# Optimization experiments

Hardware: AMD Instinct MI355X
Metric: run time of the kernel (lower is better)

Reference implementation:

```python
import jax, jax.numpy as jnp
import numpy as np

N, C, HI, WI = 8, 3, 512, 512   # src_img NCHW (input_img_size)
HO, WO = 2048, 2048             # output canvas (output_img_size[2:])
EPS = 1e-8


def _transform_one(img, coor_row):
    """Replicates: sigmoid box params -> theta -> F.affine_grid -> F.grid_sample
    (bilinear, zeros padding, align_corners=False). Theta has zero off-diagonals,
    so the grid is separable in x/y and the bilinear sample factorizes.
    img: [C, HI, WI]; coor_row: [4]. Returns (sample [C,HO,WO], mask [HO,WO])."""
    x = jax.nn.sigmoid(coor_row[0]) * WO
    y = jax.nn.sigmoid(coor_row[1]) * HO
    w = jax.nn.sigmoid(coor_row[2]) * WO
    h = jax.nn.sigmoid(coor_row[3]) * HO
    a = WO / (w + EPS)
    tx = 2.0 / WO * (WO / 2.0 - x) * a
    b = HO / (h + EPS)
    ty = 2.0 / HO * (HO / 2.0 - y) * b
    # affine_grid base coords (align_corners=False): center-of-pixel normalized
    xs = (2.0 * jnp.arange(WO, dtype=img.dtype) + 1.0) / WO - 1.0
    ys = (2.0 * jnp.arange(HO, dtype=img.dtype) + 1.0) / HO - 1.0
    gx = a * xs + tx          # [WO]
    gy = b * ys + ty          # [HO]
    # grid_sample unnormalize (align_corners=False)
    ix = ((gx + 1.0) * WI - 1.0) / 2.0
    iy = ((gy + 1.0) * HI - 1.0) / 2.0
    x0f = jnp.floor(ix); y0f = jnp.floor(iy)
    wx1 = ix - x0f; wx0 = 1.0 - wx1
    wy1 = iy - y0f; wy0 = 1.0 - wy1
    x0 = x0f.astype(jnp.int32); x1 = x0 + 1
    y0 = y0f.astype(jnp.int32); y1 = y0 + 1
    vx0 = ((x0 >= 0) & (x0 < WI)).astype(img.dtype)
    vx1 = ((x1 >= 0) & (x1 < WI)).astype(img.dtype)
    vy0 = ((y0 >= 0) & (y0 < HI)).astype(img.dtype)
    vy1 = ((y1 >= 0) & (y1 < HI)).astype(img.dtype)
    x0c = jnp.clip(x0, 0, WI - 1); x1c = jnp.clip(x1, 0, WI - 1)
    y0c = jnp.clip(y0, 0, HI - 1); y1c = jnp.clip(y1, 0, HI - 1)
    wyv0 = wy0 * vy0; wyv1 = wy1 * vy1
    wxv0 = wx0 * vx0; wxv1 = wx1 * vx1
    # separable bilinear gather with zero padding
    rows = img[:, y0c, :] * wyv0[None, :, None] + img[:, y1c, :] * wyv1[None, :, None]  # [C,HO,WI]
    samp = rows[:, :, x0c] * wxv0[None, None, :] + rows[:, :, x1c] * wxv1[None, None, :]  # [C,HO,WO]
    # grid_sample of an all-ones mask == sum of in-bounds bilinear weights (separable)
    mask = (wyv0 + wyv1)[:, None] * (wxv0 + wxv1)[None, :]  # [HO,WO]
    return samp, mask


def _composite(src_img, bg_img, coor):
    def step(bg, inp):
        img, c = inp
        s, m = _transform_one(img, c)
        bg = bg * (1.0 - m)[None, None] + (s * m[None])[None]
        return bg, None
    bg, _ = jax.lax.scan(step, bg_img, (src_img, coor))
    return bg


def setup_inputs() -> dict:
    key = jax.random.key(0)
    k1, k2, k3 = jax.random.split(key, 3)
    src_img = jax.random.normal(k1, (N, C, HI, WI), dtype=jnp.float32)
    bg_img = jax.random.uniform(k2, (1, C, HO, WO), dtype=jnp.float32)
    coor = jax.random.normal(k3, (N, 4), dtype=jnp.float32)  # nn.Parameter
    return {"src_img": src_img, "bg_img": bg_img, "coor": coor}


def reference(src_img, bg_img, coor):
    return _composite(src_img, bg_img, coor)
```

## Files before the change

kernel.cpp:

```cpp
#include <hip/hip_runtime.h>

#define WI 512
#define HI 512
#define WO 2048
#define HO 2048
#define NIMG 8
#define CCH 3
#define EPS 1e-8f
#define PLANE (HI * WI)

#define SEG  512
#define TPB  128
#define PXT  4
#define MAXR 516

struct ImgUni {
    float wy0, wy1, my;
    int   y0o, y1o;
    int   t0, t1;
};

__device__ __forceinline__ bool img_uniforms(const float4 P, const float ys,
                                             const int wo0, ImgUni& u) {
    const float gy  = P.z * ys + P.w;
    const float iy  = ((gy + 1.0f) * (float)HI - 1.0f) * 0.5f;
    const float y0f = floorf(iy);
    const float fy1 = iy - y0f;
    const float fy0 = 1.0f - fy1;
    const float y1f = y0f + 1.0f;
    const float v0  = (y0f >= 0.0f && y0f < (float)HI) ? 1.0f : 0.0f;
    const float v1  = (y1f >= 0.0f && y1f < (float)HI) ? 1.0f : 0.0f;
    u.wy0 = fy0 * v0;
    u.wy1 = fy1 * v1;
    u.my  = u.wy0 + u.wy1;
    u.y0o = (int)fminf(fmaxf(y0f, 0.0f), (float)(HI - 1)) * WI;
    u.y1o = (int)fminf(fmaxf(y1f, 0.0f), (float)(HI - 1)) * WI;
    if (!(u.my > 0.0f)) return false;

    const float a  = P.x, tx = P.y;
    const float xsf = (2.0f * (float)wo0 + 1.0f) / (float)WO - 1.0f;
    const float xsl = (2.0f * (float)(wo0 + SEG - 1) + 1.0f) / (float)WO - 1.0f;
    const float ixf = ((a * xsf + tx + 1.0f) * (float)WI - 1.0f) * 0.5f;
    const float ixl = ((a * xsl + tx + 1.0f) * (float)WI - 1.0f) * 0.5f;
    if (ixl <= -1.0f || ixf >= (float)WI) return false;
    u.t0 = (int)fminf(fmaxf(floorf(ixf), 0.0f), (float)(WI - 1));
    u.t1 = (int)fminf(fmaxf(floorf(ixl) + 1.0f, 0.0f), (float)(WI - 1));
    return true;
}

__launch_bounds__(TPB)
__global__ void diffcomp_fused7(const float* __restrict__ src,
                                const float* __restrict__ bg,
                                const float* __restrict__ coor,
                                float* __restrict__ out) {
    __shared__ float  cs[2][CCH][MAXR];
    __shared__ float4 prm[NIMG];

    const int tid = threadIdx.x;
    const int b   = blockIdx.x;
    const int row = b >> 2;
    const int wo0 = (b & 3) * SEG;

    if (tid < NIMG) {
        const float cx  = coor[tid * 4 + 0];
        const float cy  = coor[tid * 4 + 1];
        const float cw  = coor[tid * 4 + 2];
        const float chh = coor[tid * 4 + 3];
        const float x = (1.0f / (1.0f + expf(-cx))) * (float)WO;
        const float y = (1.0f / (1.0f + expf(-cy))) * (float)HO;
        const float w = (1.0f / (1.0f + expf(-cw))) * (float)WO;
        const float h = (1.0f / (1.0f + expf(-chh))) * (float)HO;
        const float a  = (float)WO / (w + EPS);
        const float tx = (2.0f / (float)WO) * ((float)WO * 0.5f - x) * a;
        const float bb = (float)HO / (h + EPS);
        const float ty = (2.0f / (float)HO) * ((float)HO * 0.5f - y) * bb;
        prm[tid] = make_float4(a, tx, bb, ty);
    }
    __syncthreads();

    const float ys = (2.0f * (float)row + 1.0f) / (float)HO - 1.0f;

    unsigned cov = 0u;
#pragma unroll
    for (int n = 0; n < NIMG; n++) {
        ImgUni u;
        if (img_uniforms(prm[n], ys, wo0, u)) cov |= (1u << n);
    }

    const int base = row * WO + wo0 + tid;
    float acc[CCH][PXT];
#pragma unroll
    for (int c = 0; c < CCH; c++)
#pragma unroll
        for (int p = 0; p < PXT; p++)
            acc[c][p] = bg[c * HO * WO + base + p * TPB];

    if (cov) {
        auto stage = [&](int slot, int n) {
            ImgUni u;
            img_uniforms(prm[n], ys, wo0, u);
            const float* ib = src + n * (CCH * PLANE);
            const int R = u.t1 - u.t0 + 1;
            for (int i = tid; i < R; i += TPB) {
#pragma unroll
                for (int c = 0; c < CCH; c++) {
                    const float r0 = ib[c * PLANE + u.y0o + u.t0 + i];
                    const float r1 = ib[c * PLANE + u.y1o + u.t0 + i];
                    cs[slot][c][i] = r0 * u.wy0 + r1 * u.wy1;
                }
            }
        };

        auto blend = [&](int slot, int n) {
            ImgUni u;
            img_uniforms(prm[n], ys, wo0, u);
            const float a  = prm[n].x;
            const float tx = prm[n].y;
            const int lim = u.t1 - u.t0;
#pragma unroll
            for (int p = 0; p < PXT; p++) {
                const int wo = wo0 + p * TPB + tid;
                const float xs  = (2.0f * (float)wo + 1.0f) / (float)WO - 1.0f;
                const float gx  = a * xs + tx;
                const float ix  = ((gx + 1.0f) * (float)WI - 1.0f) * 0.5f;
                const float x0f = floorf(ix);
                const float fx1 = ix - x0f;
                const float fx0 = 1.0f - fx1;
                const float x1f = x0f + 1.0f;
                const float v0  = (x0f >= 0.0f && x0f < (float)WI) ? 1.0f : 0.0f;
                const float v1  = (x1f >= 0.0f && x1f < (float)WI) ? 1.0f : 0.0f;
                const float wx0 = fx0 * v0;
                const float wx1 = fx1 * v1;
                int x0r = (int)fminf(fmaxf(x0f, 0.0f), (float)(WI - 1)) - u.t0;
                int x1r = (int)fminf(fmaxf(x1f, 0.0f), (float)(WI - 1)) - u.t0;
                x0r = min(max(x0r, 0), lim);
                x1r = min(max(x1r, 0), lim);
                const float m  = u.my * (wx0 + wx1);
                const float om = 1.0f - m;
#pragma unroll
                for (int c = 0; c < CCH; c++) {
                    const float q0 = cs[slot][c][x0r];
                    const float q1 = cs[slot][c][x1r];
                    const float sc = q0 * wx0 + q1 * wx1;
                    acc[c][p] = acc[c][p] * om + sc * m;
                }
            }
        };

        int cur = (int)__builtin_ctz(cov);
        unsigned rest = cov & (cov - 1u);

        stage(0, cur);
        __syncthreads();

        int s = 0;
        while (true) {
            const int nxt = rest ? (int)__builtin_ctz(rest) : -1;
            if (nxt >= 0) stage(s ^ 1, nxt);
            blend(s, cur);
            __syncthreads();
            if (nxt < 0) break;
            cur = nxt;
            rest &= rest - 1u;
            s ^= 1;
        }
    }

#pragma unroll
    for (int c = 0; c < CCH; c++)
#pragma unroll
        for (int p = 0; p < PXT; p++)
            out[c * HO * WO + base + p * TPB] = acc[c][p];
}

extern "C" void kernel_launch(void* const* d_in, const int* in_sizes, int n_in,
                              void* d_out, int out_size, void* d_ws, size_t ws_size,
                              hipStream_t stream) {
    const float* src  = (const float*)d_in[0];
    const float* bg   = (const float*)d_in[1];
    const float* coor = (const float*)d_in[2];
    float* out = (float*)d_out;
    (void)d_ws; (void)ws_size;

    hipLaunchKernelGGL(diffcomp_fused7, dim3(HO * 4), dim3(TPB), 0, stream,
                       src, bg, coor, out);
}
```

Baseline: 151.6 us.

## Prefetch source rows into registers with float4 loads and widen blocks to half-rows

Each block now covers 1024 output pixels with 256 threads instead of 512 with 128. Source-row staging uses 16-byte aligned float4 loads into registers, and the next image's rows are prefetched while the current image is committed and blended. The column x-coordinates are precomputed once per thread. This aims to cut global-load instruction count and hide load latency, at the cost of more registers and a wider, 4-aligned staging window. There is also a possible race: a slot is rewritten in the next iteration while other threads may still be blending from it, since there is no barrier after the blend.

After: 134.3 us. 11.4% less time.

```diff
diff --git a/kernel.cpp b/kernel.cpp
--- a/kernel.cpp
+++ b/kernel.cpp
@@ -9,19 +9,21 @@
 #define EPS 1e-8f
 #define PLANE (HI * WI)
 
-#define SEG  512
-#define TPB  128
+#define TPB  256
+#define SEG  1024
 #define PXT  4
-#define MAXR 516
-
-struct ImgUni {
+#define CAP  520
+
+struct SState {
     float wy0, wy1, my;
-    int   y0o, y1o;
-    int   t0, t1;
+    int   t0a, R, lim;
+    int   valid;
 };
 
-__device__ __forceinline__ bool img_uniforms(const float4 P, const float ys,
-                                             const int wo0, ImgUni& u) {
+__device__ __forceinline__ SState calc_state(const float4 P, const float ys,
+                                             const int wo0) {
+    SState st; st.valid = 0; st.wy0 = st.wy1 = st.my = 0.0f;
+    st.t0a = 0; st.R = 0; st.lim = 0;
     const float gy  = P.z * ys + P.w;
     const float iy  = ((gy + 1.0f) * (float)HI - 1.0f) * 0.5f;
     const float y0f = floorf(iy);
@@ -30,36 +32,41 @@
     const float y1f = y0f + 1.0f;
     const float v0  = (y0f >= 0.0f && y0f < (float)HI) ? 1.0f : 0.0f;
     const float v1  = (y1f >= 0.0f && y1f < (float)HI) ? 1.0f : 0.0f;
-    u.wy0 = fy0 * v0;
-    u.wy1 = fy1 * v1;
-    u.my  = u.wy0 + u.wy1;
-    u.y0o = (int)fminf(fmaxf(y0f, 0.0f), (float)(HI - 1)) * WI;
-    u.y1o = (int)fminf(fmaxf(y1f, 0.0f), (float)(HI - 1)) * WI;
-    if (!(u.my > 0.0f)) return false;
+    st.wy0 = fy0 * v0;
+    st.wy1 = fy1 * v1;
+    st.my  = st.wy0 + st.wy1;
+    if (!(st.my > 0.0f)) return st;
 
     const float a  = P.x, tx = P.y;
     const float xsf = (2.0f * (float)wo0 + 1.0f) / (float)WO - 1.0f;
     const float xsl = (2.0f * (float)(wo0 + SEG - 1) + 1.0f) / (float)WO - 1.0f;
     const float ixf = ((a * xsf + tx + 1.0f) * (float)WI - 1.0f) * 0.5f;
     const float ixl = ((a * xsl + tx + 1.0f) * (float)WI - 1.0f) * 0.5f;
-    if (ixl <= -1.0f || ixf >= (float)WI) return false;
-    u.t0 = (int)fminf(fmaxf(floorf(ixf), 0.0f), (float)(WI - 1));
-    u.t1 = (int)fminf(fmaxf(floorf(ixl) + 1.0f, 0.0f), (float)(WI - 1));
-    return true;
+    if (ixl <= -1.0f || ixf >= (float)WI) return st;
+
+    const int t0 = (int)fminf(fmaxf(floorf(ixf), 0.0f), (float)(WI - 1));
+    const int t1 = (int)fminf(fmaxf(floorf(ixl) + 1.0f, 0.0f), (float)(WI - 1));
+    st.t0a = t0 & ~3;
+    int R = (t1 - st.t0a + 4) & ~3;
+    if (R > WI - st.t0a) R = WI - st.t0a;
+    st.R   = R;
+    st.lim = t1 - st.t0a;
+    st.valid = 1;
+    return st;
 }
 
 __launch_bounds__(TPB)
-__global__ void diffcomp_fused7(const float* __restrict__ src,
-                                const float* __restrict__ bg,
-                                const float* __restrict__ coor,
-                                float* __restrict__ out) {
-    __shared__ float  cs[2][CCH][MAXR];
+__global__ void diffcomp_v8(const float* __restrict__ src,
+                            const float* __restrict__ bg,
+                            const float* __restrict__ coor,
+                            float* __restrict__ out) {
+    __shared__ float  cs[2][CCH][CAP];
     __shared__ float4 prm[NIMG];
 
     const int tid = threadIdx.x;
     const int b   = blockIdx.x;
-    const int row = b >> 2;
-    const int wo0 = (b & 3) * SEG;
+    const int row = b >> 1;
+    const int wo0 = (b & 1) << 10;
 
     if (tid < NIMG) {
         const float cx  = coor[tid * 4 + 0];
@@ -83,8 +90,14 @@
     unsigned cov = 0u;
 #pragma unroll
     for (int n = 0; n < NIMG; n++) {
-        ImgUni u;
-        if (img_uniforms(prm[n], ys, wo0, u)) cov |= (1u << n);
+        if (calc_state(prm[n], ys, wo0).valid) cov |= (1u << n);
+    }
+
+    float xsv[PXT];
+#pragma unroll
+    for (int p = 0; p < PXT; p++) {
+        const int wo = wo0 + p * TPB + tid;
+        xsv[p] = (2.0f * (float)wo + 1.0f) / (float)WO - 1.0f;
     }
 
     const int base = row * WO + wo0 + tid;
@@ -96,32 +109,49 @@
             acc[c][p] = bg[c * HO * WO + base + p * TPB];
 
     if (cov) {
-        auto stage = [&](int slot, int n) {
-            ImgUni u;
-            img_uniforms(prm[n], ys, wo0, u);
-            const float* ib = src + n * (CCH * PLANE);
-            const int R = u.t1 - u.t0 + 1;
-            for (int i = tid; i < R; i += TPB) {
+        float4 A0[CCH], A1[CCH], B0[CCH], B1[CCH];
+        SState stA, stB;
+
+        auto load_img = [&](int n, SState& st, float4* r0, float4* r1) {
+            st = calc_state(prm[n], ys, wo0);
+            const int xo = tid << 2;
+            if (xo < st.R) {
+                const float* ib = src + n * (CCH * PLANE) + st.t0a + xo;
+                const float gy  = prm[n].z * ys + prm[n].w;
+                const float iy  = ((gy + 1.0f) * (float)HI - 1.0f) * 0.5f;
+                const float y0f = floorf(iy);
+                const int y0o = (int)fminf(fmaxf(y0f, 0.0f), (float)(HI - 1)) * WI;
+                const int y1o = (int)fminf(fmaxf(y0f + 1.0f, 0.0f), (float)(HI - 1)) * WI;
 #pragma unroll
                 for (int c = 0; c < CCH; c++) {
-                    const float r0 = ib[c * PLANE + u.y0o + u.t0 + i];
-                    const float r1 = ib[c * PLANE + u.y1o + u.t0 + i];
-                    cs[slot][c][i] = r0 * u.wy0 + r1 * u.wy1;
+                    r0[c] = *(const float4*)(ib + c * PLANE + y0o);
+                    r1[c] = *(const float4*)(ib + c * PLANE + y1o);
                 }
             }
         };
 
-        auto blend = [&](int slot, int n) {
-            ImgUni u;
-            img_uniforms(prm[n], ys, wo0, u);
+        auto commit_img = [&](int slot, const SState& st,
+                              const float4* r0, const float4* r1) {
+            const int xo = tid << 2;
+            if (xo < st.R) {
+#pragma unroll
+                for (int c = 0; c < CCH; c++) {
+                    float4 rc;
+                    rc.x = r0[c].x * st.wy0 + r1[c].x * st.wy1;
+                    rc.y = r0[c].y * st.wy0 + r1[c].y * st.wy1;
+                    rc.z = r0[c].z * st.wy0 + r1[c].z * st.wy1;
+                    rc.w = r0[c].w * st.wy0 + r1[c].w * st.wy1;
+                    *(float4*)&cs[slot][c][xo] = rc;
+                }
+            }
+        };
+
+        auto blend_img = [&](int slot, int n, const SState& st) {
             const float a  = prm[n].x;
             const float tx = prm[n].y;
-            const int lim = u.t1 - u.t0;
 #pragma unroll
             for (int p = 0; p < PXT; p++) {
-                const int wo = wo0 + p * TPB + tid;
-                const float xs  = (2.0f * (float)wo + 1.0f) / (float)WO - 1.0f;
-                const float gx  = a * xs + tx;
+                const float gx  = a * xsv[p] + tx;
                 const float ix  = ((gx + 1.0f) * (float)WI - 1.0f) * 0.5f;
                 const float x0f = floorf(ix);
                 const float fx1 = ix - x0f;
@@ -131,11 +161,11 @@
                 const float v1  = (x1f >= 0.0f && x1f < (float)WI) ? 1.0f : 0.0f;
                 const float wx0 = fx0 * v0;
                 const float wx1 = fx1 * v1;
-                int x0r = (int)fminf(fmaxf(x0f, 0.0f), (float)(WI - 1)) - u.t0;
-                int x1r = (int)fminf(fmaxf(x1f, 0.0f), (float)(WI - 1)) - u.t0;
-                x0r = min(max(x0r, 0), lim);
-                x1r = min(max(x1r, 0), lim);
-                const float m  = u.my * (wx0 + wx1);
+                int x0r = (int)fminf(fmaxf(x0f, 0.0f), (float)(WI - 1)) - st.t0a;
+                int x1r = (int)fminf(fmaxf(x1f, 0.0f), (float)(WI - 1)) - st.t0a;
+                x0r = min(max(x0r, 0), st.lim);
+                x1r = min(max(x1r, 0), st.lim);
+                const float m  = st.my * (wx0 + wx1);
                 const float om = 1.0f - m;
 #pragma unroll
                 for (int c = 0; c < CCH; c++) {
@@ -150,18 +180,20 @@
         int cur = (int)__builtin_ctz(cov);
         unsigned rest = cov & (cov - 1u);
 
-        stage(0, cur);
-        __syncthreads();
-
+        load_img(cur, stA, A0, A1);
         int s = 0;
         while (true) {
             const int nxt = rest ? (int)__builtin_ctz(rest) : -1;
-            if (nxt >= 0) stage(s ^ 1, nxt);
-            blend(s, cur);
+            if (nxt >= 0) load_img(nxt, stB, B0, B1);
+            commit_img(s, stA, A0, A1);
             __syncthreads();
+            blend_img(s, cur, stA);
             if (nxt < 0) break;
             cur = nxt;
             rest &= rest - 1u;
+            stA = stB;
+#pragma unroll
+            for (int c = 0; c < CCH; c++) { A0[c] = B0[c]; A1[c] = B1[c]; }
             s ^= 1;
         }
     }
@@ -182,6 +214,6 @@
     float* out = (float*)d_out;
     (void)d_ws; (void)ws_size;
 
-    hipLaunchKernelGGL(diffcomp_fused7, dim3(HO * 4), dim3(TPB), 0, stream,
+    hipLaunchKernelGGL(diffcomp_v8, dim3(HO * (WO / SEG)), dim3(TPB), 0, stream,
                        src, bg, coor, out);
 }
```
